# Optimization experiments

Hardware: AMD Instinct MI355X
Metric: run time of the kernel (lower is better)

Reference implementation:

```python
import jax, jax.numpy as jnp
import numpy as np

B, T, TRAIN = 4, 2048, 1536
D, H, L, FF, V = 512, 8, 12, 2048, 100
DH = D // H
ROPE_BASE = 100000.0


def layer_norm(x, g, b, eps=1e-5):
    mu = jnp.mean(x, axis=-1, keepdims=True)
    var = jnp.mean(jnp.square(x - mu), axis=-1, keepdims=True)
    return (x - mu) * jax.lax.rsqrt(var + eps) * g + b


def rope_cos_sin(t, dh):
    inv_freq = 1.0 / (ROPE_BASE ** (jnp.arange(0, dh, 2, dtype=jnp.float32) / dh))  # (dh/2,)
    ang = jnp.arange(t, dtype=jnp.float32)[:, None] * inv_freq[None, :]  # (T, dh/2)
    return jnp.cos(ang), jnp.sin(ang)


def apply_rope_interleaved(x, cos, sin):
    # x: (B, T, H, DH); interleaved pairs (x0,x1),(x2,x3),...
    x1, x2 = x[..., 0::2], x[..., 1::2]
    c, s = cos[None, :, None, :], sin[None, :, None, :]
    r1 = x1 * c - x2 * s
    r2 = x1 * s + x2 * c
    return jnp.stack([r1, r2], axis=-1).reshape(x.shape)


def setup_inputs() -> dict:
    key = jax.random.key(0)
    ks = jax.random.split(key, 20)
    sc = 0.02
    inp = {
        'R': jax.random.normal(ks[0], (B, T, D), jnp.float32),
        'y_train': jax.random.randint(ks[1], (B, TRAIN), 0, V),
        'emb': jax.random.normal(ks[2], (V, D), jnp.float32) * sc,
        'Wqkv': jax.random.normal(ks[3], (L, D, 3 * D), jnp.float32) * sc,
        'bqkv': jnp.zeros((L, 3 * D), jnp.float32),
        'Wo': jax.random.normal(ks[4], (L, D, D), jnp.float32) * sc,
        'bo': jnp.zeros((L, D), jnp.float32),
        'ln1_g': jnp.ones((L, D), jnp.float32),
        'ln1_b': jnp.zeros((L, D), jnp.float32),
        'ln2_g': jnp.ones((L, D), jnp.float32),
        'ln2_b': jnp.zeros((L, D), jnp.float32),
        'W1': jax.random.normal(ks[5], (L, D, FF), jnp.float32) * sc,
        'b1': jnp.zeros((L, FF), jnp.float32),
        'W2': jax.random.normal(ks[6], (L, FF, D), jnp.float32) * sc,
        'b2': jnp.zeros((L, D), jnp.float32),
        'pW1': jax.random.normal(ks[7], (D, 2 * D), jnp.float32) * sc,
        'pb1': jnp.zeros((2 * D,), jnp.float32),
        'pW2': jax.random.normal(ks[8], (2 * D, V), jnp.float32) * sc,
        'pb2': jnp.zeros((V,), jnp.float32),
    }
    return inp


def icl_forward(R, y_train, emb, Wqkv, bqkv, Wo, bo, ln1_g, ln1_b, ln2_g, ln2_b, W1, b1, W2, b2, pW1, pb1, pW2, pb2):
    b, t, d = R.shape
    train = y_train.shape[1]
    # label embedding: train rows get emb[y], test rows get zeros
    y_emb = jnp.concatenate([emb[y_train], jnp.zeros((b, t - train, d), R.dtype)], axis=1)
    rep = R + y_emb
    # ICL mask: column j visible iff j < train or j == i
    idx = jnp.arange(t)
    allowed = (idx[None, :] < train) | (idx[:, None] == idx[None, :])
    mask = jnp.where(allowed, 0.0, -jnp.inf).astype(R.dtype)  # (T, T)
    cos, sin = rope_cos_sin(t, DH)
    scale = 1.0 / jnp.sqrt(jnp.asarray(DH, R.dtype))

    def block(x, p):
        wqkv, bq, wo, bob, g1, be1, g2, be2, w1, bb1, w2, bb2 = p
        h = layer_norm(x, g1, be1)
        qkv = h @ wqkv + bq  # (B,T,3D)
        q, k, v = jnp.split(qkv, 3, axis=-1)
        q = q.reshape(b, t, H, DH)
        k = k.reshape(b, t, H, DH)
        v = v.reshape(b, t, H, DH)
        q = apply_rope_interleaved(q, cos, sin)
        k = apply_rope_interleaved(k, cos, sin)
        scores = jnp.einsum('bthd,bshd->bhts', q, k) * scale + mask
        attn = jax.nn.softmax(scores, axis=-1)
        o = jnp.einsum('bhts,bshd->bthd', attn, v).reshape(b, t, d)
        x = x + o @ wo + bob
        h2 = layer_norm(x, g2, be2)
        x = x + jax.nn.gelu(h2 @ w1 + bb1) @ w2 + bb2
        return x, None

    rep, _ = jax.lax.scan(block, rep, (Wqkv, bqkv, Wo, bo, ln1_g, ln1_b, ln2_g, ln2_b, W1, b1, W2, b2))
    test = rep[:, train:, :]
    logits = jax.nn.gelu(test @ pW1 + pb1) @ pW2 + pb2  # (B, test, V)
    return logits


def reference(R, y_train, emb, Wqkv, bqkv, Wo, bo, ln1_g, ln1_b, ln2_g, ln2_b, W1, b1, W2, b2, pW1, pb1, pW2, pb2):
    return icl_forward(R, y_train, emb, Wqkv, bqkv, Wo, bo, ln1_g, ln1_b, ln2_g, ln2_b, W1, b1, W2, b2, pW1, pb1, pW2, pb2)
```

## Files before the change

kernel.cpp:

```cpp
#include <hip/hip_runtime.h>
#include <hip/hip_bf16.h>

#define BB 4
#define TT 2048
#define TRAIN 1536
#define DD 512
#define HH 8
#define LL 12
#define FFD 2048
#define VV 100
#define DH 64
#define NT (BB*TT)
#define NTEST (BB*(TT-TRAIN))

typedef __bf16 bf16x8 __attribute__((ext_vector_type(8)));
typedef float  f32x4  __attribute__((ext_vector_type(4)));
typedef unsigned int u32x4 __attribute__((ext_vector_type(4)));

#define GLDS16(g, l) __builtin_amdgcn_global_load_lds( \
    (const __attribute__((address_space(1))) void*)(g), \
    (__attribute__((address_space(3))) void*)(l), 16, 0, 0)

__global__ __launch_bounds__(256) void emb_add(const float* __restrict__ R,
                                               const int* __restrict__ y,
                                               const float* __restrict__ emb,
                                               float* __restrict__ rep) {
    int idx = blockIdx.x * 256 + threadIdx.x;
    int d = idx & 511;
    int n = idx >> 9;
    int t = n & (TT - 1);
    int b = n >> 11;
    float val = R[idx];
    if (t < TRAIN) {
        int tok = y[b * TRAIN + t];
        val += emb[(size_t)tok * DD + d];
    }
    rep[idx] = val;
}

__global__ __launch_bounds__(256) void ln_wave(const float* __restrict__ x,
                                               const float* __restrict__ g,
                                               const float* __restrict__ bta,
                                               __bf16* __restrict__ out) {
    int row = blockIdx.x * 4 + (threadIdx.x >> 6);
    int lane = threadIdx.x & 63;
    const float* xr = x + (size_t)row * DD + lane * 8;
    float4 a = *(const float4*)xr;
    float4 c = *(const float4*)(xr + 4);
    float s  = a.x + a.y + a.z + a.w + c.x + c.y + c.z + c.w;
    float sq = a.x*a.x + a.y*a.y + a.z*a.z + a.w*a.w + c.x*c.x + c.y*c.y + c.z*c.z + c.w*c.w;
#pragma unroll
    for (int off = 1; off < 64; off <<= 1) {
        s  += __shfl_xor(s, off);
        sq += __shfl_xor(sq, off);
    }
    float mu  = s * (1.0f / DD);
    float var = sq * (1.0f / DD) - mu * mu;
    float inv = rsqrtf(var + 1e-5f);
    const float* gp = g + lane * 8;
    const float* bp = bta + lane * 8;
    float4 g0 = *(const float4*)gp, g1 = *(const float4*)(gp + 4);
    float4 b0 = *(const float4*)bp, b1 = *(const float4*)(bp + 4);
    __bf16 o8[8];
    o8[0] = (__bf16)((a.x - mu) * inv * g0.x + b0.x);
    o8[1] = (__bf16)((a.y - mu) * inv * g0.y + b0.y);
    o8[2] = (__bf16)((a.z - mu) * inv * g0.z + b0.z);
    o8[3] = (__bf16)((a.w - mu) * inv * g0.w + b0.w);
    o8[4] = (__bf16)((c.x - mu) * inv * g1.x + b1.x);
    o8[5] = (__bf16)((c.y - mu) * inv * g1.y + b1.y);
    o8[6] = (__bf16)((c.z - mu) * inv * g1.z + b1.z);
    o8[7] = (__bf16)((c.w - mu) * inv * g1.w + b1.w);
    *(uint4*)(out + (size_t)row * DD + lane * 8) = *(uint4*)o8;
}

__global__ __launch_bounds__(256) void rope_tab(float* __restrict__ ctab, float* __restrict__ stab) {
    int idx = blockIdx.x * 256 + threadIdx.x;
    int p = idx & 31, t = idx >> 5;
    double freq = exp(-((double)(2 * p) / 64.0) * log(100000.0));
    double ang = (double)t * freq;
    ctab[idx] = (float)cos(ang);
    stab[idx] = (float)sin(ang);
}

__global__ __launch_bounds__(256) void rope_vt(const __bf16* __restrict__ qkv,
                                               const float* __restrict__ ctab,
                                               const float* __restrict__ stab,
                                               __bf16* __restrict__ qo,
                                               __bf16* __restrict__ ko,
                                               __bf16* __restrict__ vt) {
    int bh = blockIdx.y; int b = bh >> 3, h = bh & 7;
    int t0 = blockIdx.x * 64;
    __shared__ __bf16 tile[64][72];
    int tid = threadIdx.x;
    {
        int r = tid >> 2, cg = (tid & 3) * 16;
        const __bf16* src = qkv + (size_t)(b * TT + t0 + r) * (3 * DD) + 2 * DD + h * DH + cg;
        *(uint4*)&tile[r][cg]     = *(const uint4*)&src[0];
        *(uint4*)&tile[r][cg + 8] = *(const uint4*)&src[8];
    }
#pragma unroll
    for (int c = 0; c < 2; ++c) {
        int lin = c * 256 + tid;
        int tl = lin >> 3, u = lin & 7;
        int t = t0 + tl;
        const __bf16* base = qkv + (size_t)(b * TT + t) * (3 * DD) + h * DH + u * 8;
        uint4 qu = *(const uint4*)base;
        uint4 ku = *(const uint4*)(base + DD);
        float4 cv = *(const float4*)(ctab + t * 32 + u * 4);
        float4 sv = *(const float4*)(stab + t * 32 + u * 4);
        const __bf16* qp = (const __bf16*)&qu;
        const __bf16* kp = (const __bf16*)&ku;
        float cc[4] = {cv.x, cv.y, cv.z, cv.w};
        float ss[4] = {sv.x, sv.y, sv.z, sv.w};
        __bf16 oq[8], ok8[8];
#pragma unroll
        for (int j = 0; j < 4; ++j) {
            float x1 = (float)qp[2 * j], x2 = (float)qp[2 * j + 1];
            float k1 = (float)kp[2 * j], k2 = (float)kp[2 * j + 1];
            oq[2 * j]     = (__bf16)((x1 * cc[j] - x2 * ss[j]) * 0.125f);
            oq[2 * j + 1] = (__bf16)((x1 * ss[j] + x2 * cc[j]) * 0.125f);
            ok8[2 * j]     = (__bf16)(k1 * cc[j] - k2 * ss[j]);
            ok8[2 * j + 1] = (__bf16)(k1 * ss[j] + k2 * cc[j]);
        }
        size_t ob = ((size_t)bh * TT + t) * DH + u * 8;
        *(uint4*)(qo + ob) = *(uint4*)oq;
        *(uint4*)(ko + ob) = *(uint4*)ok8;
    }
    __syncthreads();
    {
        int dh = tid >> 2, tg = (tid & 3) * 16;
        __bf16 outv[16];
#pragma unroll
        for (int j = 0; j < 16; ++j) outv[j] = tile[tg + j][dh];
        __bf16* dst = vt + ((size_t)bh * DH + dh) * TT + t0 + tg;
        *(uint4*)&dst[0] = *(uint4*)&outv[0];
        *(uint4*)&dst[8] = *(uint4*)&outv[8];
    }
}

#define NCH (TRAIN/128)

__global__ __launch_bounds__(256, 2) void attn_mfma(const __bf16* __restrict__ q,
                                                    const __bf16* __restrict__ k,
                                                    const __bf16* __restrict__ vt,
                                                    __bf16* __restrict__ obuf) {
    __shared__ __align__(16) __bf16 Kb[2][128 * 64];
    __shared__ __align__(16) __bf16 Vb[2][64 * 128];
    __shared__ float sself[128];

    const int tid = threadIdx.x;
    const int lin = blockIdx.x;
    const int xcd = lin & 7, sblk = lin >> 3;
    const int bh = xcd * 4 + (sblk & 3);
    const int t0q = (sblk >> 2) * 128;
    const int b = bh >> 3, hh = bh & 7;
    const size_t kbase = (size_t)bh * TT * DH;
    const int w = tid >> 6;
    const int lane = tid & 63;
    const int l16 = lane & 15;
    const int quad = lane >> 4;
    const int x7 = l16 & 7;

    bf16x8 qa[2][2];
#pragma unroll
    for (int mi = 0; mi < 2; ++mi)
#pragma unroll
        for (int ks = 0; ks < 2; ++ks) {
            const __bf16* qg = q + kbase + (size_t)(t0q + w * 32 + mi * 16 + l16) * DH + ks * 32 + quad * 8;
            qa[mi][ks] = *(const bf16x8*)qg;
        }

    const int krl = lane >> 3, ksl = lane & 7;
    const int vrl = lane >> 4, vsl = lane & 15;

    f32x4 oa[2][4] = {};
    float lsum[2] = {0.f, 0.f};

    {
#pragma unroll
        for (int c = 0; c < 4; ++c) {
            int rb = w * 4 + c;
            GLDS16(k + kbase + (size_t)(rb * 8 + krl) * DH + ((ksl ^ krl) * 8), &Kb[0][rb * 512]);
            int dh = rb * 4 + vrl;
            GLDS16(vt + kbase + (size_t)dh * TT + ((vsl ^ (dh & 7)) * 8), &Vb[0][rb * 512]);
        }
    }

    for (int ci = 0; ci < NCH; ++ci) {
        __syncthreads();
        if (ci + 1 < NCH) {
            const __bf16* gk = k + kbase + (size_t)((ci + 1) * 128) * DH;
            __bf16* dK = Kb[(ci + 1) & 1];
            __bf16* dV = Vb[(ci + 1) & 1];
#pragma unroll
            for (int c = 0; c < 4; ++c) {
                int rb = w * 4 + c;
                GLDS16(gk + (size_t)(rb * 8 + krl) * DH + ((ksl ^ krl) * 8), dK + rb * 512);
                int dh = rb * 4 + vrl;
                GLDS16(vt + kbase + (size_t)dh * TT + (ci + 1) * 128 + ((vsl ^ (dh & 7)) * 8), dV + rb * 512);
            }
        }

        const __bf16* kc = Kb[ci & 1];
        f32x4 acc[2][8] = {};
        __builtin_amdgcn_s_setprio(1);
#pragma unroll
        for (int ks = 0; ks < 2; ++ks) {
            bf16x8 kf[8];
#pragma unroll
            for (int ni = 0; ni < 8; ++ni)
                kf[ni] = *(const bf16x8*)&kc[(ni * 16 + l16) * 64 + (((ks * 4 + quad) ^ x7) * 8)];
#pragma unroll
            for (int ni = 0; ni < 8; ++ni) {
                acc[0][ni] = __builtin_amdgcn_mfma_f32_16x16x32_bf16(kf[ni], qa[0][ks], acc[0][ni], 0, 0, 0);
                acc[1][ni] = __builtin_amdgcn_mfma_f32_16x16x32_bf16(kf[ni], qa[1][ks], acc[1][ni], 0, 0, 0);
            }
        }
        __builtin_amdgcn_s_setprio(0);

        u32x4 pa[2][4];
#pragma unroll
        for (int mi = 0; mi < 2; ++mi) {
            unsigned int pk[8][2];
            float rs = 0.f;
#pragma unroll
            for (int ni = 0; ni < 8; ++ni) {
                float p0 = __expf(acc[mi][ni][0]);
                float p1 = __expf(acc[mi][ni][1]);
                float p2 = __expf(acc[mi][ni][2]);
                float p3 = __expf(acc[mi][ni][3]);
                rs += (p0 + p1) + (p2 + p3);
                asm("v_cvt_pk_bf16_f32 %0, %1, %2" : "=v"(pk[ni][0]) : "v"(p0), "v"(p1));
                asm("v_cvt_pk_bf16_f32 %0, %1, %2" : "=v"(pk[ni][1]) : "v"(p2), "v"(p3));
            }
            rs += __shfl_xor(rs, 16);
            rs += __shfl_xor(rs, 32);
            lsum[mi] += rs;
#pragma unroll
            for (int ks = 0; ks < 4; ++ks)
#pragma unroll
                for (int rr = 0; rr < 2; ++rr) {
                    unsigned int A = pk[2 * ks][rr], Bv = pk[2 * ks + 1][rr];
                    asm("v_permlane32_swap_b32 %0, %1" : "+v"(A), "+v"(Bv));
                    asm("v_permlane16_swap_b32 %0, %1" : "+v"(A), "+v"(Bv));
                    pa[mi][ks][rr]     = A;
                    pa[mi][ks][rr + 2] = Bv;
                }
        }

        const __bf16* vc = Vb[ci & 1];
        __builtin_amdgcn_s_setprio(1);
#pragma unroll
        for (int ks = 0; ks < 4; ++ks) {
            bf16x8 vf[4];
#pragma unroll
            for (int ni = 0; ni < 4; ++ni)
                vf[ni] = *(const bf16x8*)&vc[(ni * 16 + l16) * 128 + (((ks * 4 + quad) ^ x7) * 8)];
            bf16x8 pa0, pa1;
            { u32x4 t = pa[0][ks]; __builtin_memcpy(&pa0, &t, 16); }
            { u32x4 t = pa[1][ks]; __builtin_memcpy(&pa1, &t, 16); }
#pragma unroll
            for (int ni = 0; ni < 4; ++ni) {
                oa[0][ni] = __builtin_amdgcn_mfma_f32_16x16x32_bf16(pa0, vf[ni], oa[0][ni], 0, 0, 0);
                oa[1][ni] = __builtin_amdgcn_mfma_f32_16x16x32_bf16(pa1, vf[ni], oa[1][ni], 0, 0, 0);
            }
        }
        __builtin_amdgcn_s_setprio(0);
    }

    float lr[2][4];
#pragma unroll
    for (int mi = 0; mi < 2; ++mi)
#pragma unroll
        for (int r = 0; r < 4; ++r)
            lr[mi][r] = __shfl(lsum[mi], quad * 4 + r);

    if (t0q >= TRAIN) {
        __syncthreads();
        {
            int dh = tid >> 2, cg = (tid & 3) * 32;
            const __bf16* vg = vt + kbase + (size_t)dh * TT + t0q + cg;
#pragma unroll
            for (int u = 0; u < 4; ++u)
                *(uint4*)&Vb[0][dh * 128 + cg + u * 8] = *(const uint4*)&vg[u * 8];
            int row = tid >> 1, hf = tid & 1;
            const __bf16* qp = q + kbase + (size_t)(t0q + row) * DH + hf * 32;
            const __bf16* kp = k + kbase + (size_t)(t0q + row) * DH + hf * 32;
            float dacc = 0.f;
#pragma unroll
            for (int u = 0; u < 4; ++u) {
                uint4 uq = *(const uint4*)&qp[u * 8];
                uint4 uk = *(const uint4*)&kp[u * 8];
                const __bf16* pq = (const __bf16*)&uq;
                const __bf16* pk2 = (const __bf16*)&uk;
#pragma unroll
                for (int j = 0; j < 8; ++j) dacc += (float)pq[j] * (float)pk2[j];
            }
            dacc += __shfl_xor(dacc, 1);
            sself[row] = dacc;
        }
        __syncthreads();
#pragma unroll
        for (int mi = 0; mi < 2; ++mi)
#pragma unroll
            for (int r = 0; r < 4; ++r) {
                int qr = w * 32 + mi * 16 + quad * 4 + r;
                float pp = __expf(sself[qr]);
                lr[mi][r] += pp;
#pragma unroll
                for (int ni = 0; ni < 4; ++ni)
                    oa[mi][ni][r] += pp * (float)Vb[0][(ni * 16 + l16) * 128 + qr];
            }
    }

#pragma unroll
    for (int mi = 0; mi < 2; ++mi)
#pragma unroll
        for (int r = 0; r < 4; ++r) {
            float inv = 1.f / lr[mi][r];
            int trow = t0q + w * 32 + mi * 16 + quad * 4 + r;
            __bf16* op = obuf + ((size_t)(b * TT) + trow) * DD + hh * 64;
#pragma unroll
            for (int ni = 0; ni < 4; ++ni)
                op[ni * 16 + l16] = (__bf16)(oa[mi][ni][r] * inv);
        }
}

__global__ __launch_bounds__(256) void transpose_pad(const float* __restrict__ src,
                                                     __bf16* __restrict__ dst,
                                                     int K, int N) {
    __shared__ __bf16 t[32][33];
    int n0 = blockIdx.x * 32, k0 = blockIdx.y * 32;
    int tx = threadIdx.x & 31, ty = threadIdx.x >> 5;
#pragma unroll
    for (int i = 0; i < 4; ++i) {
        int nn = n0 + tx;
        t[ty + i * 8][tx] = (nn < N) ? (__bf16)src[(size_t)(k0 + ty + i * 8) * N + nn] : (__bf16)0.f;
    }
    __syncthreads();
#pragma unroll
    for (int i = 0; i < 4; ++i) {
        dst[(size_t)(n0 + ty + i * 8) * K + k0 + tx] = t[tx][ty + i * 8];
    }
}

__global__ __launch_bounds__(256) void transpose_all(const float* __restrict__ s0,
                                                     const float* __restrict__ s1,
                                                     const float* __restrict__ s2,
                                                     const float* __restrict__ s3,
                                                     __bf16* __restrict__ d0, __bf16* __restrict__ d1,
                                                     __bf16* __restrict__ d2, __bf16* __restrict__ d3) {
    int i = blockIdx.x;
    const float* src; __bf16* dst; int K, N, tx, ty;
    if (i < 768)       { src = s0; dst = d0; K = 512;  N = 1536; int j = i;        tx = j % 48; ty = j / 48; }
    else if (i < 1024) { src = s1; dst = d1; K = 512;  N = 512;  int j = i - 768;  tx = j % 16; ty = j / 16; }
    else if (i < 2048) { src = s2; dst = d2; K = 512;  N = 2048; int j = i - 1024; tx = j % 64; ty = j / 64; }
    else               { src = s3; dst = d3; K = 2048; N = 512;  int j = i - 2048; tx = j % 16; ty = j / 16; }
    __shared__ __bf16 t[32][33];
    int n0 = tx * 32, k0 = ty * 32;
    int lx = threadIdx.x & 31, ly = threadIdx.x >> 5;
#pragma unroll
    for (int c = 0; c < 4; ++c)
        t[ly + c * 8][lx] = (__bf16)src[(size_t)(k0 + ly + c * 8) * N + n0 + lx];
    __syncthreads();
#pragma unroll
    for (int c = 0; c < 4; ++c)
        dst[(size_t)(n0 + ly + c * 8) * K + k0 + lx] = t[lx][ly + c * 8];
}

template <int EP, int TN>
__global__ __launch_bounds__(256, 2) void gemm_bt(const __bf16* __restrict__ A,
                                                  const __bf16* __restrict__ Bt,
                                                  const float* __restrict__ bias,
                                                  float* __restrict__ resid,
                                                  __bf16* __restrict__ Cout,
                                                  int M, int N, int K) {
    constexpr int NI = TN / 32;
    constexpr int BC = TN / 32;
    __shared__ __align__(16) __bf16 As[2][128 * 64];
    __shared__ __align__(16) __bf16 Bs[2][TN * 64];
    const int tid = threadIdx.x;
    const int gx = gridDim.x;
    const int linb = blockIdx.x + gx * blockIdx.y;
    const int xs = gx >> 3;
    const int xcd = linb & 7, sb = linb >> 3;
    const int bx = xcd * xs + (sb % xs);
    const int by = sb / xs;
    const int m0 = bx * 128;
    const int n0 = by * TN;
    const int lane = tid & 63;
    const int w = tid >> 6;
    const int wm = (w >> 1) * 64, wn = (w & 1) * (TN / 2);
    const int lrow = lane & 15;
    const int quad = lane >> 4;
    const int x7 = lrow & 7;

    f32x4 acc[4][NI] = {};

    const int sr = lane >> 3;
    const int sc = ((lane & 7) ^ sr) * 8;
    const __bf16* gA = A  + (size_t)(m0 + w * 32 + sr) * K + sc;
    const __bf16* gB = Bt + (size_t)(n0 + w * (TN / 4) + sr) * K + sc;

    auto stage = [&](int kt, int buf) {
        const int k0 = kt << 6;
#pragma unroll
        for (int c = 0; c < 4; ++c)
            GLDS16(gA + (size_t)(c * 8) * K + k0, &As[buf][(w * 32 + c * 8) * 64]);
#pragma unroll
        for (int c = 0; c < BC; ++c)
            GLDS16(gB + (size_t)(c * 8) * K + k0, &Bs[buf][(w * (TN / 4) + c * 8) * 64]);
    };

    const int nk = K >> 6;
    stage(0, 0);
    for (int kt = 0; kt < nk; ++kt) {
        __syncthreads();
        if (kt + 1 < nk) stage(kt + 1, (kt + 1) & 1);
        const __bf16* as = As[kt & 1];
        const __bf16* bs = Bs[kt & 1];
#pragma unroll
        for (int ks = 0; ks < 2; ++ks) {
            bf16x8 afr[4], bfr[NI];
#pragma unroll
            for (int i = 0; i < 4; ++i)
                afr[i] = *(const bf16x8*)&as[(wm + i * 16 + lrow) * 64 + (((ks * 4 + quad) ^ x7) * 8)];
#pragma unroll
            for (int i = 0; i < NI; ++i)
                bfr[i] = *(const bf16x8*)&bs[(wn + i * 16 + lrow) * 64 + (((ks * 4 + quad) ^ x7) * 8)];
#pragma unroll
            for (int mi = 0; mi < 4; ++mi)
#pragma unroll
                for (int ni = 0; ni < NI; ++ni)
                    acc[mi][ni] = __builtin_amdgcn_mfma_f32_16x16x32_bf16(afr[mi], bfr[ni], acc[mi][ni], 0, 0, 0);
        }
    }

    const int crow = (lane >> 4) * 4;
    const int ccol = lane & 15;
#pragma unroll
    for (int mi = 0; mi < 4; ++mi) {
#pragma unroll
        for (int ni = 0; ni < NI; ++ni) {
            int gn = n0 + wn + ni * 16 + ccol;
            float bv = bias[gn];
#pragma unroll
            for (int r = 0; r < 4; ++r) {
                int gm = m0 + wm + mi * 16 + crow + r;
                float vvv = acc[mi][ni][r] + bv;
                if constexpr (EP == 1) {
                    float x = vvv;
                    vvv = x / (1.f + __expf(-1.5957691216f * (x + 0.044715f * x * x * x)));
                }
                if constexpr (EP == 2) {
                    resid[(size_t)gm * N + gn] += vvv;
                } else if constexpr (EP == 4) {
                    if (gn < VV) resid[(size_t)gm * VV + gn] = vvv;
                } else {
                    Cout[(size_t)gm * N + gn] = (__bf16)vvv;
                }
            }
        }
    }
}

__global__ __launch_bounds__(256) void cast_test(const float* __restrict__ rep, __bf16* __restrict__ testb) {
    int idx = blockIdx.x * 256 + threadIdx.x;
    int d = idx & 511;
    int i = idx >> 9;
    int ttk = i & 511;
    int b = i >> 9;
    testb[idx] = (__bf16)rep[(size_t)(b * TT + TRAIN + ttk) * DD + d];
}

__global__ void pad_bias(const float* __restrict__ pb2, float* __restrict__ pb2p) {
    int t = threadIdx.x;
    if (t < 128) pb2p[t] = (t < VV) ? pb2[t] : 0.f;
}

extern "C" void kernel_launch(void* const* d_in, const int* in_sizes, int n_in,
                              void* d_out, int out_size, void* d_ws, size_t ws_size,
                              hipStream_t stream) {
    const float* R    = (const float*)d_in[0];
    const int*   y    = (const int*)d_in[1];
    const float* emb  = (const float*)d_in[2];
    const float* Wqkv = (const float*)d_in[3];
    const float* bqkv = (const float*)d_in[4];
    const float* Wo   = (const float*)d_in[5];
    const float* bo   = (const float*)d_in[6];
    const float* ln1g = (const float*)d_in[7];
    const float* ln1b = (const float*)d_in[8];
    const float* ln2g = (const float*)d_in[9];
    const float* ln2b = (const float*)d_in[10];
    const float* W1   = (const float*)d_in[11];
    const float* b1   = (const float*)d_in[12];
    const float* W2   = (const float*)d_in[13];
    const float* b2   = (const float*)d_in[14];
    const float* pW1  = (const float*)d_in[15];
    const float* pb1  = (const float*)d_in[16];
    const float* pW2  = (const float*)d_in[17];
    const float* pb2  = (const float*)d_in[18];

    char* p = (char*)d_ws;
    float* rep    = (float*)p;  p += (size_t)NT * DD * 4;
    __bf16* hbuf  = (__bf16*)p; p += (size_t)NT * DD * 2;
    __bf16* qkv   = (__bf16*)p;
    __bf16* ffb   = qkv;        p += (size_t)NT * FFD * 2;
    __bf16* qb    = (__bf16*)p; p += (size_t)NT * DD * 2;
    __bf16* kb    = (__bf16*)p; p += (size_t)NT * DD * 2;
    __bf16* vtb   = (__bf16*)p; p += (size_t)NT * DD * 2;
    __bf16* obuf  = (__bf16*)p; p += (size_t)NT * DD * 2;
    __bf16* wqkvT = (__bf16*)p; p += (size_t)1536 * 512 * 2;
    __bf16* woT   = (__bf16*)p; p += (size_t)512 * 512 * 2;
    __bf16* w1T   = (__bf16*)p; p += (size_t)2048 * 512 * 2;
    __bf16* w2T   = (__bf16*)p; p += (size_t)512 * 2048 * 2;
    float* ctab   = (float*)p;  p += (size_t)TT * 32 * 4;
    float* stab   = (float*)p;  p += (size_t)TT * 32 * 4;
    float* pb2p   = (float*)p;  p += 512;
    __bf16* testb = hbuf;
    __bf16* hb    = obuf;

    emb_add<<<NT * DD / 256, 256, 0, stream>>>(R, y, emb, rep);
    rope_tab<<<TT * 32 / 256, 256, 0, stream>>>(ctab, stab);

    for (int l = 0; l < LL; ++l) {
        ln_wave<<<NT / 4, 256, 0, stream>>>(rep, ln1g + l * DD, ln1b + l * DD, hbuf);
        transpose_all<<<3072, 256, 0, stream>>>(Wqkv + (size_t)l * DD * 3 * DD, Wo + (size_t)l * DD * DD,
                                                W1 + (size_t)l * DD * FFD, W2 + (size_t)l * FFD * DD,
                                                wqkvT, woT, w1T, w2T);
        gemm_bt<0, 128><<<dim3(NT / 128, 1536 / 128), 256, 0, stream>>>(hbuf, wqkvT, bqkv + l * 3 * DD, nullptr, qkv, NT, 3 * DD, DD);
        rope_vt<<<dim3(TT / 64, BB * HH), 256, 0, stream>>>(qkv, ctab, stab, qb, kb, vtb);
        attn_mfma<<<dim3(512), 256, 0, stream>>>(qb, kb, vtb, obuf);
        gemm_bt<2, 128><<<dim3(NT / 128, 512 / 128), 256, 0, stream>>>(obuf, woT, bo + l * DD, rep, nullptr, NT, DD, DD);
        ln_wave<<<NT / 4, 256, 0, stream>>>(rep, ln2g + l * DD, ln2b + l * DD, hbuf);
        gemm_bt<1, 128><<<dim3(NT / 128, FFD / 128), 256, 0, stream>>>(hbuf, w1T, b1 + l * FFD, nullptr, ffb, NT, FFD, DD);
        gemm_bt<2, 128><<<dim3(NT / 128, 512 / 128), 256, 0, stream>>>(ffb, w2T, b2 + l * DD, rep, nullptr, NT, DD, FFD);
    }

    cast_test<<<NTEST * DD / 256, 256, 0, stream>>>(rep, testb);
    transpose_pad<<<dim3(1024 / 32, 512 / 32), 256, 0, stream>>>(pW1, w1T, DD, 2 * DD);
    gemm_bt<1, 64><<<dim3(NTEST / 128, 1024 / 64), 256, 0, stream>>>(testb, w1T, pb1, nullptr, hb, NTEST, 2 * DD, DD);
    pad_bias<<<1, 128, 0, stream>>>(pb2, pb2p);
    transpose_pad<<<dim3(128 / 32, 1024 / 32), 256, 0, stream>>>(pW2, w2T, 2 * DD, VV);
    gemm_bt<4, 128><<<dim3(NTEST / 128, 1), 256, 0, stream>>>(hb, w2T, pb2p, (float*)d_out, nullptr, NTEST, 128, 2 * DD);
}
```

Measured before the change: 2.494 ms.

## Use triple-buffered K=32 GEMM pipeline with vmcnt waits and MFMA-native LDS layout

The bf16 GEMM now stages K-tiles of 32 instead of 64, into three LDS buffers with two tiles in flight. It waits on explicit vmcnt counts plus a raw s_barrier instead of a full __syncthreads. The LDS layout is rearranged so each lane's 16-byte fragment is read contiguously without the XOR swizzle. Launch bounds are raised to three blocks per CU, since each block now uses less LDS. The aim is deeper overlap of global-to-LDS loads with MFMA work and higher occupancy, at the cost of more barriers per unit of K and hand-counted vmcnt values that must match the number of issued loads.

```diff
diff --git a/kernel.cpp b/kernel.cpp
--- a/kernel.cpp
+++ b/kernel.cpp
@@ -368,17 +368,19 @@
         dst[(size_t)(n0 + ly + c * 8) * K + k0 + lx] = t[lx][ly + c * 8];
 }
 
+#define WAITVM(n) asm volatile("s_waitcnt vmcnt(" #n ")" ::: "memory")
+
 template <int EP, int TN>
-__global__ __launch_bounds__(256, 2) void gemm_bt(const __bf16* __restrict__ A,
+__global__ __launch_bounds__(256, 3) void gemm_bt(const __bf16* __restrict__ A,
                                                   const __bf16* __restrict__ Bt,
                                                   const float* __restrict__ bias,
                                                   float* __restrict__ resid,
                                                   __bf16* __restrict__ Cout,
                                                   int M, int N, int K) {
     constexpr int NI = TN / 32;
-    constexpr int BC = TN / 32;
-    __shared__ __align__(16) __bf16 As[2][128 * 64];
-    __shared__ __align__(16) __bf16 Bs[2][TN * 64];
+    constexpr int BCALL = TN / 64;
+    __shared__ __align__(16) __bf16 As[3][128 * 32];
+    __shared__ __align__(16) __bf16 Bs[3][TN * 32];
     const int tid = threadIdx.x;
     const int gx = gridDim.x;
     const int linb = blockIdx.x + gx * blockIdx.y;
@@ -391,53 +393,60 @@
     const int lane = tid & 63;
     const int w = tid >> 6;
     const int wm = (w >> 1) * 64, wn = (w & 1) * (TN / 2);
-    const int lrow = lane & 15;
+    const int l16 = lane & 15;
     const int quad = lane >> 4;
-    const int x7 = lrow & 7;
 
     f32x4 acc[4][NI] = {};
 
-    const int sr = lane >> 3;
-    const int sc = ((lane & 7) ^ sr) * 8;
-    const __bf16* gA = A  + (size_t)(m0 + w * 32 + sr) * K + sc;
-    const __bf16* gB = Bt + (size_t)(n0 + w * (TN / 4) + sr) * K + sc;
+    const __bf16* gA = A  + (size_t)(m0 + w * 32 + l16) * K + quad * 8;
+    const __bf16* gB = Bt + (size_t)(n0 + w * (TN / 4) + l16) * K + quad * 8;
 
     auto stage = [&](int kt, int buf) {
-        const int k0 = kt << 6;
-#pragma unroll
-        for (int c = 0; c < 4; ++c)
-            GLDS16(gA + (size_t)(c * 8) * K + k0, &As[buf][(w * 32 + c * 8) * 64]);
-#pragma unroll
-        for (int c = 0; c < BC; ++c)
-            GLDS16(gB + (size_t)(c * 8) * K + k0, &Bs[buf][(w * (TN / 4) + c * 8) * 64]);
+        const int k0 = kt << 5;
+#pragma unroll
+        for (int c = 0; c < 2; ++c)
+            GLDS16(gA + (size_t)(c * 16) * K + k0, &As[buf][(w * 32 + c * 16) * 32]);
+#pragma unroll
+        for (int c = 0; c < BCALL; ++c)
+            GLDS16(gB + (size_t)(c * 16) * K + k0, &Bs[buf][(w * (TN / 4) + c * 16) * 32]);
     };
 
-    const int nk = K >> 6;
+    const int nk = K >> 5;
     stage(0, 0);
+    stage(1, 1);
+    int buf = 0;
     for (int kt = 0; kt < nk; ++kt) {
-        __syncthreads();
-        if (kt + 1 < nk) stage(kt + 1, (kt + 1) & 1);
-        const __bf16* as = As[kt & 1];
-        const __bf16* bs = Bs[kt & 1];
-#pragma unroll
-        for (int ks = 0; ks < 2; ++ks) {
+        if (kt < nk - 1) {
+            if constexpr (TN == 128) WAITVM(4); else WAITVM(3);
+        } else {
+            WAITVM(0);
+        }
+        __builtin_amdgcn_s_barrier();
+        if (kt + 2 < nk) {
+            int b2 = buf + 2; if (b2 >= 3) b2 -= 3;
+            stage(kt + 2, b2);
+        }
+        const __bf16* as = As[buf];
+        const __bf16* bs = Bs[buf];
+        {
             bf16x8 afr[4], bfr[NI];
 #pragma unroll
             for (int i = 0; i < 4; ++i)
-                afr[i] = *(const bf16x8*)&as[(wm + i * 16 + lrow) * 64 + (((ks * 4 + quad) ^ x7) * 8)];
+                afr[i] = *(const bf16x8*)&as[((wm >> 4) + i) * 512 + quad * 128 + l16 * 8];
 #pragma unroll
             for (int i = 0; i < NI; ++i)
-                bfr[i] = *(const bf16x8*)&bs[(wn + i * 16 + lrow) * 64 + (((ks * 4 + quad) ^ x7) * 8)];
+                bfr[i] = *(const bf16x8*)&bs[((wn >> 4) + i) * 512 + quad * 128 + l16 * 8];
 #pragma unroll
             for (int mi = 0; mi < 4; ++mi)
 #pragma unroll
                 for (int ni = 0; ni < NI; ++ni)
                     acc[mi][ni] = __builtin_amdgcn_mfma_f32_16x16x32_bf16(afr[mi], bfr[ni], acc[mi][ni], 0, 0, 0);
         }
-    }
-
-    const int crow = (lane >> 4) * 4;
-    const int ccol = lane & 15;
+        ++buf; if (buf == 3) buf = 0;
+    }
+
+    const int crow = quad * 4;
+    const int ccol = l16;
 #pragma unroll
     for (int mi = 0; mi < 4; ++mi) {
 #pragma unroll
```

New measurement: 3.093 ms. +24.0%, slower.
